# Performance work log

Hardware: AMD Instinct MI355X
Metric: run time of the kernel (lower is better)

The kernel has to match this reference:

```python
import jax, jax.numpy as jnp
import numpy as np

N, T, D, H = 256, 128, 512, 1024


def setup_inputs() -> dict:
    key = jax.random.key(0)
    k_x, k_A, k_Wx, k_Wh, k_Wa = jax.random.split(key, 5)
    x = jax.random.normal(k_x, (N, T, D), dtype=jnp.float32)
    A = jax.random.normal(k_A, (N, H, 4, 4), dtype=jnp.float32)
    Wx = jax.random.normal(k_Wx, (D, 4 * H), dtype=jnp.float32) / np.sqrt(D)
    Wh = jax.random.normal(k_Wh, (H, 4 * H), dtype=jnp.float32) / np.sqrt(H)
    Wattn = jax.random.normal(k_Wa, (H, 4 * H), dtype=jnp.float32) / np.sqrt(H)
    b = jnp.zeros((4 * H,), dtype=jnp.float32)
    return {"x": x, "A": A, "Wx": Wx, "Wh": Wh, "Wattn": Wattn, "b": b}


def _attention_lstm(x, A, Wx, Wh, Wattn, b):
    # A: (N, H, 4, 4) -> flatten spatial to (N, H, 16)
    A_flat = A.reshape(A.shape[0], A.shape[1], -1)
    h0 = A_flat.mean(axis=2)  # (N, H)
    c0 = h0
    Hdim = h0.shape[1]
    scale = 1.0 / jnp.sqrt(jnp.asarray(Hdim, dtype=x.dtype))

    def step(carry, x_t):
        prev_h, prev_c = carry
        # scaled dot-product attention over 16 spatial locations
        scores = jnp.einsum("nh,nhs->ns", prev_h, A_flat) * scale  # (N, 16)
        w = jax.nn.softmax(scores, axis=1)
        attn = jnp.einsum("nhs,ns->nh", A_flat, w)  # (N, H)
        # fused LSTM gates
        a = x_t @ Wx + prev_h @ Wh + attn @ Wattn + b  # (N, 4H)
        i = jax.nn.sigmoid(a[:, 0:Hdim])
        f = jax.nn.sigmoid(a[:, Hdim:2 * Hdim])
        o = jax.nn.sigmoid(a[:, 2 * Hdim:3 * Hdim])
        g = jnp.tanh(a[:, 3 * Hdim:4 * Hdim])
        next_c = f * prev_c + i * g
        next_h = o * jnp.tanh(next_c)
        return (next_h, next_c), next_h

    x_tnd = jnp.swapaxes(x, 0, 1)  # (T, N, D)
    _, h_tnh = jax.lax.scan(step, (h0, c0), x_tnd)
    return jnp.swapaxes(h_tnh, 0, 1)  # (N, T, H)


def reference(x, A, Wx, Wh, Wattn, b):
    return _attention_lstm(x, A, Wx, Wh, Wattn, b)
```

## Files before the change

### kernel.cpp

```cpp
#include <hip/hip_runtime.h>
#include <math.h>

#define NB 256
#define TT 128
#define DD 512
#define HH 1024
#define KHX 1536
#define KFB 2560
#define BK 128
#define NBLK5 256
#define NHALF 128

typedef _Float16 half_t;
typedef _Float16 half8 __attribute__((ext_vector_type(8)));
typedef _Float16 half4v __attribute__((ext_vector_type(4)));
typedef _Float16 half2v __attribute__((ext_vector_type(2)));
typedef float f32x4 __attribute__((ext_vector_type(4)));


__global__ __launch_bounds__(256) void k_trans(const float* __restrict__ src,
        half_t* __restrict__ dst, int kstride, int koff, int nkt) {
    __shared__ half_t tile[64][65];
    int bk = blockIdx.x % nkt;
    int bn = blockIdx.x / nkt;
    int k0 = bk * 64, n0 = bn * 64;
    #pragma unroll
    for (int i = 0; i < 16; ++i) {
        int idx = i * 256 + threadIdx.x;
        int r = idx >> 6, c = idx & 63;
        tile[c][r] = (half_t)src[(size_t)(k0 + r) * 4096 + n0 + c];
    }
    __syncthreads();
    #pragma unroll
    for (int i = 0; i < 16; ++i) {
        int idx = i * 256 + threadIdx.x;
        int r = idx >> 6, c = idx & 63;
        dst[(size_t)(n0 + r) * kstride + koff + k0 + c] = tile[r][c];
    }
}

__global__ __launch_bounds__(256) void k_convX(const float* __restrict__ x,
        half_t* __restrict__ x16) {
    size_t base = ((size_t)blockIdx.x * 256 + threadIdx.x) * 32;
    #pragma unroll
    for (int u = 0; u < 4; ++u) {
        float4 a = ((const float4*)(x + base))[2 * u];
        float4 c = ((const float4*)(x + base))[2 * u + 1];
        half8 p;
        p[0] = (half_t)a.x; p[1] = (half_t)a.y; p[2] = (half_t)a.z; p[3] = (half_t)a.w;
        p[4] = (half_t)c.x; p[5] = (half_t)c.y; p[6] = (half_t)c.z; p[7] = (half_t)c.w;
        ((half8*)(x16 + base))[u] = p;
    }
}

__global__ __launch_bounds__(256) void k_convA2(const float* __restrict__ A,
        half_t* __restrict__ A16, half_t* __restrict__ AsT,
        float* __restrict__ cbuf, half_t* __restrict__ h16) {
    int n = blockIdx.x, tid = threadIdx.x;
    #pragma unroll
    for (int r = 0; r < 4; ++r) {
        int h = tid + r * 256;
        const float4* ap = (const float4*)(A + ((size_t)n * HH + h) * 16);
        float4 v0 = ap[0], v1 = ap[1], v2 = ap[2], v3 = ap[3];
        float a[16];
        a[0]=v0.x; a[1]=v0.y; a[2] =v0.z; a[3] =v0.w;
        a[4]=v1.x; a[5]=v1.y; a[6] =v1.z; a[7] =v1.w;
        a[8]=v2.x; a[9]=v2.y; a[10]=v2.z; a[11]=v2.w;
        a[12]=v3.x; a[13]=v3.y; a[14]=v3.z; a[15]=v3.w;
        float hv = 0.f;
        #pragma unroll
        for (int s = 0; s < 16; ++s) hv += a[s];
        hv *= (1.f / 16.f);
        size_t ci = (size_t)n * HH + h;
        cbuf[ci] = hv;
        h16[ci] = (half_t)hv;
        half8 q0, q1;
        #pragma unroll
        for (int s = 0; s < 8; ++s) { q0[s] = (half_t)a[s]; q1[s] = (half_t)a[s + 8]; }
        *(half8*)(A16 + ci * 16) = q0;
        *(half8*)(A16 + ci * 16 + 8) = q1;
        #pragma unroll
        for (int s = 0; s < 16; ++s)
            AsT[(size_t)n * 16 * HH + (size_t)s * HH + h] = (half_t)a[s];
    }
}

__global__ __launch_bounds__(256) void k_initsc(const half_t* __restrict__ h16,
        const half_t* __restrict__ A16,
        float* __restrict__ sc0, float* __restrict__ sc1, float* __restrict__ sc2) {
    __shared__ float sred[4][16];
    int n = blockIdx.x, tid = threadIdx.x;
    float ps[16];
    #pragma unroll
    for (int s = 0; s < 16; ++s) ps[s] = 0.f;
    #pragma unroll
    for (int r = 0; r < 4; ++r) {
        int h = tid + r * 256;
        size_t ci = (size_t)n * HH + h;
        float hv = (float)h16[ci];
        const half8* ap = (const half8*)(A16 + ci * 16);
        half8 a0 = ap[0], a1 = ap[1];
        #pragma unroll
        for (int s = 0; s < 8; ++s) {
            ps[s]     += hv * (float)a0[s];
            ps[s + 8] += hv * (float)a1[s];
        }
    }
    #pragma unroll
    for (int off = 32; off; off >>= 1)
        #pragma unroll
        for (int s = 0; s < 16; ++s) ps[s] += __shfl_xor(ps[s], off, 64);
    int wave = tid >> 6;
    if ((tid & 63) == 0)
        #pragma unroll
        for (int s = 0; s < 16; ++s) sred[wave][s] = ps[s];
    __syncthreads();
    if (tid < 16)
        sc0[(size_t)n * 16 + tid] =
            sred[0][tid] + sred[1][tid] + sred[2][tid] + sred[3][tid];
    if (tid < 112) {
        int x = 1 + tid / 16, s = tid % 16;
        sc0[((size_t)x * 256 + n) * 16 + s] = 0.f;
    }
    if (tid < 128) {
        int x = tid / 16, s = tid % 16;
        sc1[((size_t)x * 256 + n) * 16 + s] = 0.f;
        sc2[((size_t)x * 256 + n) * 16 + s] = 0.f;
    }
}

__global__ __launch_bounds__(256) void k_gemm_G(const half_t* __restrict__ AsT,
        const half_t* __restrict__ WaT, half_t* __restrict__ G16) {
    __shared__ half_t sAs[16][BK + 8];
    __shared__ half_t sB[4][16][BK + 8];
    int bid = blockIdx.x;
    int n = bid >> 6, jt = bid & 63;
    int j0 = jt * 16;
    int tid = threadIdx.x, wv = tid >> 6, lane = tid & 63;
    f32x4 acc = {};
    int srB = tid >> 2, scB = (tid & 3) * 32;
    int gB = srB >> 4, jcB = srB & 15;
    for (int it = 0; it < HH / BK; ++it) {
        int k0 = it * BK;
        if (tid < 128) {
            int r = tid >> 3, c = (tid & 7) * 16;
            const uint4* sp = (const uint4*)(AsT + (size_t)n * 16 * HH + (size_t)r * HH + k0 + c);
            uint4 u0 = sp[0], u1 = sp[1];
            *(uint4*)&sAs[r][c] = u0;
            *(uint4*)&sAs[r][c + 8] = u1;
        }
        {
            const half_t* src = WaT + ((size_t)(gB * HH + j0 + jcB)) * HH + k0 + scB;
            uint4 u0 = ((const uint4*)src)[0];
            uint4 u1 = ((const uint4*)src)[1];
            uint4 u2 = ((const uint4*)src)[2];
            uint4 u3 = ((const uint4*)src)[3];
            *((uint4*)&sB[gB][jcB][scB])      = u0;
            *((uint4*)&sB[gB][jcB][scB + 8])  = u1;
            *((uint4*)&sB[gB][jcB][scB + 16]) = u2;
            *((uint4*)&sB[gB][jcB][scB + 24]) = u3;
        }
        __syncthreads();
        int row16 = lane & 15, kg = lane >> 4;
        #pragma unroll
        for (int kc = 0; kc < BK / 32; ++kc) {
            half8 bf = *(const half8*)&sB[wv][row16][kc * 32 + kg * 8];
            half8 af = *(const half8*)&sAs[row16][kc * 32 + kg * 8];
            acc = __builtin_amdgcn_mfma_f32_16x16x32_f16(af, bf, acc, 0, 0, 0);
        }
        __syncthreads();
    }
    int col = lane & 15, rbase = (lane >> 4) * 4;
    size_t jf = (size_t)wv * HH + j0 + col;
    half4v o;
    o[0] = (half_t)acc[0]; o[1] = (half_t)acc[1];
    o[2] = (half_t)acc[2]; o[3] = (half_t)acc[3];
    *(half4v*)(G16 + ((size_t)n * 4096 + jf) * 16 + rbase) = o;
}

__global__ __launch_bounds__(256) void k_gemm_XW(const half_t* __restrict__ x16,
        const half_t* __restrict__ WhxT, half_t* __restrict__ XW16) {
    __shared__ half_t sA[128][72];
    __shared__ half_t sB[64][72];
    int bid = blockIdx.x;
    int bm = bid & 255;
    int bj = bid >> 8;
    int row0 = bm * 128;
    int col0 = bj * 64;
    int tid = threadIdx.x, wv = tid >> 6, lane = tid & 63;
    int la = lane & 15, kg = lane >> 4;
    int mh = wv & 1, jh = wv >> 1;
    f32x4 acc[4][2] = {};
    int srA = tid >> 1, scA = (tid & 1) * 32;
    int srB = tid >> 2, scB = (tid & 3) * 16;
    for (int c = 0; c < 8; ++c) {
        {
            const uint4* sp = (const uint4*)(x16 + (size_t)(row0 + srA) * DD + c * 64 + scA);
            uint4 u0 = sp[0], u1 = sp[1];
            *(uint4*)&sA[srA][scA] = u0;
            *(uint4*)&sA[srA][scA + 8] = u1;
        }
        {
            const uint4* sp = (const uint4*)(WhxT + (size_t)(col0 + srB) * KHX + c * 64 + scB);
            *(uint4*)&sB[srB][scB] = sp[0];
        }
        __syncthreads();
        #pragma unroll
        for (int ks = 0; ks < 2; ++ks) {
            half8 b0 = *(const half8*)&sB[jh * 32 + la][ks * 32 + kg * 8];
            half8 b1 = *(const half8*)&sB[jh * 32 + 16 + la][ks * 32 + kg * 8];
            #pragma unroll
            for (int m = 0; m < 4; ++m) {
                half8 af = *(const half8*)&sA[mh * 64 + m * 16 + la][ks * 32 + kg * 8];
                acc[m][0] = __builtin_amdgcn_mfma_f32_16x16x32_f16(af, b0, acc[m][0], 0, 0, 0);
                acc[m][1] = __builtin_amdgcn_mfma_f32_16x16x32_f16(af, b1, acc[m][1], 0, 0, 0);
            }
        }
        __syncthreads();
    }
    __syncthreads();
    half_t (*Cl)[72] = sA;
    #pragma unroll
    for (int m = 0; m < 4; ++m)
        #pragma unroll
        for (int jt = 0; jt < 2; ++jt)
            #pragma unroll
            for (int q = 0; q < 4; ++q) {
                int rl = mh * 64 + m * 16 + kg * 4 + q;
                int cl = jh * 32 + jt * 16 + la;
                Cl[rl][cl] = (half_t)acc[m][jt][q];
            }
    __syncthreads();
    int g = col0 >> 10;
    #pragma unroll
    for (int i = 0; i < 4; ++i) {
        int idx = tid + i * 256;
        int rl = idx >> 3, grp = idx & 7;
        int R = row0 + rl;
        int t = R & 127, nn = R >> 7;
        int mh2 = nn >> 7, nl2 = nn & 127;
        int jb2 = ((col0 & 1023) >> 3) + grp;
        size_t dst = ((((size_t)t * 128 + jb2) * 2 + mh2) * 128 + nl2) * 32 + g * 8;
        *(half8*)(XW16 + dst) = *(const half8*)&Cl[rl][grp * 8];
    }
}


struct StepLds5 {
    half_t W[32][1028];
    union {
        float sm[4][128][16];
        struct {
            float pe[128][33];
            float pad[384];
            float ps[2][128][18];
        } e;
    } u;
};

__device__ __forceinline__ void grid_sync5(int* cnt, int* flag, int inst) {
    __syncthreads();
    if (threadIdx.x == 0) {
        __threadfence();
        int prev = __hip_atomic_fetch_add(cnt, 1, __ATOMIC_RELAXED,
                                          __HIP_MEMORY_SCOPE_AGENT);
        if (prev == NHALF * (inst + 1) - 1) {
            __hip_atomic_store(flag, inst + 1, __ATOMIC_RELAXED,
                               __HIP_MEMORY_SCOPE_AGENT);
        } else {
            int guard = 0;
            while (__hip_atomic_load(flag, __ATOMIC_RELAXED,
                                     __HIP_MEMORY_SCOPE_AGENT) < inst + 1) {
                __builtin_amdgcn_s_sleep(2);
                if (++guard > (1 << 24)) break;
            }
        }
        __threadfence();
    }
    __syncthreads();
}

__global__ __launch_bounds__(512, 1) void k_steps5(
        const half_t* __restrict__ XW16, half_t* __restrict__ h16A,
        half_t* __restrict__ h16B, const half_t* __restrict__ WhxT,
        const half_t* __restrict__ A16, const half_t* __restrict__ G16,
        const float* __restrict__ b, const float* __restrict__ cbuf,
        float* __restrict__ sc0, float* __restrict__ sc1, float* __restrict__ sc2,
        float* __restrict__ out, int* __restrict__ bar) {
    __shared__ StepLds5 L;
    int bid = blockIdx.x;
    int mhalf = bid & 1, jb = bid >> 1;
    int n0 = mhalf * 128;
    int tid = threadIdx.x;
    int wv = tid >> 6, lane = tid & 63;
    int la = lane & 15, kg = lane >> 4;
    int slice = bid & 7;
    int* cnt  = bar + mhalf * 32;
    int* flag = bar + mhalf * 32 + 16;

    {
        int wr = tid >> 4, seg = tid & 15;
        const half_t* wsrc = WhxT + (size_t)((wr >> 3) * HH + jb * 8 + (wr & 7)) * KHX
                           + DD + seg * 64;
        #pragma unroll
        for (int i = 0; i < 8; ++i)
            *(uint4*)&L.W[wr][seg * 64 + i * 8] = ((const uint4*)wsrc)[i];
    }

    int n_l = tid & 127, jg2 = tid >> 7;
    int n = n0 + n_l;
    int jbase = jb * 8 + jg2 * 2;
    half8 gq[4][4];
    #pragma unroll
    for (int g = 0; g < 4; ++g) {
        const half8* gsrc = (const half8*)(G16 + ((size_t)n * 4096 + g * HH + jbase) * 16);
        #pragma unroll
        for (int i = 0; i < 4; ++i) gq[g][i] = gsrc[i];
    }
    half8 aq[4];
    {
        const half8* asrc = (const half8*)(A16 + ((size_t)n * HH + jbase) * 16);
        #pragma unroll
        for (int i = 0; i < 4; ++i) aq[i] = asrc[i];
    }
    float bb[4][2];
    #pragma unroll
    for (int g = 0; g < 4; ++g) {
        bb[g][0] = b[g * HH + jbase];
        bb[g][1] = b[g * HH + jbase + 1];
    }
    float creg[2];
    creg[0] = cbuf[(size_t)n * HH + jbase];
    creg[1] = cbuf[(size_t)n * HH + jbase + 1];

    float* scC = sc0; float* scN = sc1; float* scZ = sc2;
    half_t* h16c = h16A;
    half_t* h16n = h16B;

    half2v xwv[4];
    {
        const half_t* xwp = XW16 + (((size_t)jb * 2 + mhalf) * 128 + n_l) * 32;
        #pragma unroll
        for (int g = 0; g < 4; ++g) xwv[g] = *(const half2v*)(xwp + g * 8 + jg2 * 2);
    }

    for (int t = 0; t < TT; ++t) {
        if (jb < 32) {
            int idx = jb * 512 + tid;
            int sl = idx >> 11, rem = idx & 2047;
            int nn = rem >> 4, s = rem & 15;
            scZ[((size_t)sl * 256 + n0 + nn) * 16 + s] = 0.f;
        }

        {
            const float* p0 = scC + ((size_t)(jg2 * 2) * 256 + n) * 16;
            const float* p1 = scC + ((size_t)(jg2 * 2 + 1) * 256 + n) * 16;
            #pragma unroll
            for (int i = 0; i < 4; ++i) {
                float4 a = ((const float4*)p0)[i];
                float4 c = ((const float4*)p1)[i];
                float4 o;
                o.x = a.x + c.x; o.y = a.y + c.y; o.z = a.z + c.z; o.w = a.w + c.w;
                *(float4*)&L.u.sm[jg2][n_l][4 * i] = o;
            }
        }
        __syncthreads();
        float w16[16];
        {
            float sc[16];
            #pragma unroll
            for (int i = 0; i < 4; ++i) {
                float4 q0 = *(const float4*)&L.u.sm[0][n_l][4 * i];
                float4 q1 = *(const float4*)&L.u.sm[1][n_l][4 * i];
                float4 q2 = *(const float4*)&L.u.sm[2][n_l][4 * i];
                float4 q3 = *(const float4*)&L.u.sm[3][n_l][4 * i];
                sc[4 * i + 0] = q0.x + q1.x + q2.x + q3.x;
                sc[4 * i + 1] = q0.y + q1.y + q2.y + q3.y;
                sc[4 * i + 2] = q0.z + q1.z + q2.z + q3.z;
                sc[4 * i + 3] = q0.w + q1.w + q2.w + q3.w;
            }
            float m = -1e30f;
            #pragma unroll
            for (int s = 0; s < 16; ++s) { sc[s] *= 0.03125f; m = fmaxf(m, sc[s]); }
            float den = 0.f;
            #pragma unroll
            for (int s = 0; s < 16; ++s) { sc[s] = expf(sc[s] - m); den += sc[s]; }
            float inv = 1.f / den;
            #pragma unroll
            for (int s = 0; s < 16; ++s) w16[s] = sc[s] * inv;
        }
        __syncthreads();

        f32x4 acc0 = {}, acc1 = {};
        {
            const half_t* hrow = h16c + (size_t)(n0 + wv * 16 + la) * HH + kg * 8;
            #pragma unroll
            for (int c = 0; c < 32; ++c) {
                half8 af = *(const half8*)(hrow + c * 32);
                half8 b0 = *(const half8*)&L.W[la][c * 32 + kg * 8];
                half8 b1 = *(const half8*)&L.W[16 + la][c * 32 + kg * 8];
                acc0 = __builtin_amdgcn_mfma_f32_16x16x32_f16(af, b0, acc0, 0, 0, 0);
                acc1 = __builtin_amdgcn_mfma_f32_16x16x32_f16(af, b1, acc1, 0, 0, 0);
            }
        }

        #pragma unroll
        for (int q = 0; q < 4; ++q) {
            L.u.e.pe[wv * 16 + kg * 4 + q][la]      = acc0[q];
            L.u.e.pe[wv * 16 + kg * 4 + q][16 + la] = acc1[q];
        }
        __syncthreads();

        float v[4][2];
        #pragma unroll
        for (int g = 0; g < 4; ++g) {
            #pragma unroll
            for (int jj = 0; jj < 2; ++jj) {
                float a0 = 0.f;
                #pragma unroll
                for (int s = 0; s < 16; ++s)
                    a0 += w16[s] * (float)gq[g][jj * 2 + (s >> 3)][s & 7];
                v[g][jj] = L.u.e.pe[n_l][g * 8 + jg2 * 2 + jj] + bb[g][jj]
                         + (float)xwv[g][jj] + a0;
            }
        }
        float hv[2];
        #pragma unroll
        for (int jj = 0; jj < 2; ++jj) {
            float ig = 1.f / (1.f + expf(-v[0][jj]));
            float fg = 1.f / (1.f + expf(-v[1][jj]));
            float og = 1.f / (1.f + expf(-v[2][jj]));
            float gg = tanhf(v[3][jj]);
            float cn = fg * creg[jj] + ig * gg;
            creg[jj] = cn;
            hv[jj] = og * tanhf(cn);
        }
        {
            float2 o2; o2.x = hv[0]; o2.y = hv[1];
            *(float2*)(out + ((size_t)n * TT + t) * HH + jbase) = o2;
            half2v h2; h2[0] = (half_t)hv[0]; h2[1] = (half_t)hv[1];
            *(half2v*)(h16n + (size_t)n * HH + jbase) = h2;
        }
        float p[16];
        #pragma unroll
        for (int s = 0; s < 16; ++s)
            p[s] = hv[0] * (float)aq[s >> 3][s & 7]
                 + hv[1] * (float)aq[2 + (s >> 3)][s & 7];
        int pair = jg2 >> 1;
        if ((jg2 & 1) == 0) {
            #pragma unroll
            for (int s = 0; s < 16; ++s) L.u.e.ps[pair][n_l][s] = p[s];
        }
        __syncthreads();
        if ((jg2 & 1) == 1) {
            #pragma unroll
            for (int s = 0; s < 16; ++s) L.u.e.ps[pair][n_l][s] += p[s];
        }
        __syncthreads();
        #pragma unroll
        for (int i = 0; i < 4; ++i) {
            int slot = tid * 4 + i;
            int nn = slot >> 4, s = slot & 15;
            atomicAdd(scN + ((size_t)slice * 256 + n0 + nn) * 16 + s,
                      L.u.e.ps[0][nn][s] + L.u.e.ps[1][nn][s]);
        }

        if (t + 1 < TT) {
            half2v xwn[4];
            const half_t* xwp = XW16 + ((((size_t)(t + 1) * 128 + jb) * 2 + mhalf) * 128 + n_l) * 32;
            #pragma unroll
            for (int g = 0; g < 4; ++g) xwn[g] = *(const half2v*)(xwp + g * 8 + jg2 * 2);
            grid_sync5(cnt, flag, t);
            #pragma unroll
            for (int g = 0; g < 4; ++g) xwv[g] = xwn[g];
        }
        float* tmp = scC; scC = scN; scN = scZ; scZ = tmp;
        half_t* th = h16c; h16c = h16n; h16n = th;
    }
}


__global__ __launch_bounds__(256) void k_convA(const float* __restrict__ A,
        half_t* __restrict__ A16, half_t* __restrict__ AsT,
        float* __restrict__ cbuf, half_t* __restrict__ h16,
        float* __restrict__ sc0, float* __restrict__ sc1, float* __restrict__ sc2) {
    __shared__ float sred[4][16];
    int n = blockIdx.x, tid = threadIdx.x;
    float ps[16];
    #pragma unroll
    for (int s = 0; s < 16; ++s) ps[s] = 0.f;
    #pragma unroll
    for (int r = 0; r < 4; ++r) {
        int h = tid + r * 256;
        const float4* ap = (const float4*)(A + ((size_t)n * HH + h) * 16);
        float4 v0 = ap[0], v1 = ap[1], v2 = ap[2], v3 = ap[3];
        float a[16];
        a[0]=v0.x; a[1]=v0.y; a[2] =v0.z; a[3] =v0.w;
        a[4]=v1.x; a[5]=v1.y; a[6] =v1.z; a[7] =v1.w;
        a[8]=v2.x; a[9]=v2.y; a[10]=v2.z; a[11]=v2.w;
        a[12]=v3.x; a[13]=v3.y; a[14]=v3.z; a[15]=v3.w;
        float hv = 0.f;
        #pragma unroll
        for (int s = 0; s < 16; ++s) hv += a[s];
        hv *= (1.f / 16.f);
        size_t ci = (size_t)n * HH + h;
        cbuf[ci] = hv;
        h16[ci] = (half_t)hv;
        half8 q0, q1;
        #pragma unroll
        for (int s = 0; s < 8; ++s) { q0[s] = (half_t)a[s]; q1[s] = (half_t)a[s + 8]; }
        *(half8*)(A16 + ci * 16) = q0;
        *(half8*)(A16 + ci * 16 + 8) = q1;
        #pragma unroll
        for (int s = 0; s < 16; ++s)
            AsT[(size_t)n * 16 * HH + (size_t)s * HH + h] = (half_t)a[s];
        #pragma unroll
        for (int s = 0; s < 16; ++s) ps[s] += hv * a[s];
    }
    #pragma unroll
    for (int off = 32; off; off >>= 1)
        #pragma unroll
        for (int s = 0; s < 16; ++s) ps[s] += __shfl_xor(ps[s], off, 64);
    int wave = tid >> 6;
    if ((tid & 63) == 0)
        #pragma unroll
        for (int s = 0; s < 16; ++s) sred[wave][s] = ps[s];
    __syncthreads();
    if (tid < 16) {
        sc0[n * 16 + tid] = sred[0][tid] + sred[1][tid] + sred[2][tid] + sred[3][tid];
        sc1[n * 16 + tid] = 0.f;
        sc2[n * 16 + tid] = 0.f;
    }
}

union LdsS {
    struct {
        half_t sA[32][BK + 8];
        half_t sB[4][16][BK + 8];
    } s;
    float pe[4][32][16];
};

__global__ __launch_bounds__(256) void k_step(const float* __restrict__ x,
        const half_t* __restrict__ h16c, half_t* __restrict__ h16n,
        const half_t* __restrict__ WhxT, const half_t* __restrict__ A16,
        const half_t* __restrict__ G16, const float* __restrict__ b,
        float* __restrict__ cbuf, const float* __restrict__ scC,
        float* __restrict__ scN, float* __restrict__ scZ,
        float* __restrict__ out, int t) {
    __shared__ LdsS L;
    __shared__ float wlds[32][16];
    int bid = blockIdx.x;
    int xcd = bid & 7, slot = bid >> 3;
    int mtile = slot & 7, jtile = slot >> 3;
    int n0 = mtile * 32;
    int j0 = xcd * 128 + jtile * 16;
    int tid = threadIdx.x, wv = tid >> 6, lane = tid & 63;

    if (bid < 16) scZ[bid * 256 + tid] = 0.f;
    if (tid < 32) {
        int n = n0 + tid;
        const float4* sp = (const float4*)(scC + n * 16);
        float4 u0 = sp[0], u1 = sp[1], u2 = sp[2], u3 = sp[3];
        float sc[16] = {u0.x, u0.y, u0.z, u0.w, u1.x, u1.y, u1.z, u1.w,
                        u2.x, u2.y, u2.z, u2.w, u3.x, u3.y, u3.z, u3.w};
        float m = -1e30f;
        #pragma unroll
        for (int s = 0; s < 16; ++s) { sc[s] *= 0.03125f; m = fmaxf(m, sc[s]); }
        float den = 0.f;
        #pragma unroll
        for (int s = 0; s < 16; ++s) { sc[s] = expf(sc[s] - m); den += sc[s]; }
        float inv = 1.f / den;
        #pragma unroll
        for (int s = 0; s < 16; ++s) wlds[tid][s] = sc[s] * inv;
    }

    f32x4 acc[2] = {};
    int srA = tid >> 3, scA = (tid & 7) * 16;
    int srB = tid >> 2, scB = (tid & 3) * 32;
    int gB = srB >> 4, jcB = srB & 15;

    for (int it = 0; it < KHX / BK; ++it) {
        int k0 = it * BK;
        {
            int n = n0 + srA;
            if (k0 < DD) {
                const float* src = x + ((size_t)n * TT + t) * DD + k0 + scA;
                float4 v0 = ((const float4*)src)[0];
                float4 v1 = ((const float4*)src)[1];
                float4 v2 = ((const float4*)src)[2];
                float4 v3 = ((const float4*)src)[3];
                half8 p0, p1;
                p0[0] = (half_t)v0.x; p0[1] = (half_t)v0.y; p0[2] = (half_t)v0.z; p0[3] = (half_t)v0.w;
                p0[4] = (half_t)v1.x; p0[5] = (half_t)v1.y; p0[6] = (half_t)v1.z; p0[7] = (half_t)v1.w;
                p1[0] = (half_t)v2.x; p1[1] = (half_t)v2.y; p1[2] = (half_t)v2.z; p1[3] = (half_t)v2.w;
                p1[4] = (half_t)v3.x; p1[5] = (half_t)v3.y; p1[6] = (half_t)v3.z; p1[7] = (half_t)v3.w;
                *(half8*)&L.s.sA[srA][scA]     = p0;
                *(half8*)&L.s.sA[srA][scA + 8] = p1;
            } else {
                const half_t* srch = h16c + (size_t)n * HH + (k0 - DD) + scA;
                uint4 u0 = ((const uint4*)srch)[0];
                uint4 u1 = ((const uint4*)srch)[1];
                *((uint4*)&L.s.sA[srA][scA])     = u0;
                *((uint4*)&L.s.sA[srA][scA + 8]) = u1;
            }
        }
        {
            const half_t* src = WhxT + ((size_t)(gB * HH + j0 + jcB)) * KHX + k0 + scB;
            uint4 u0 = ((const uint4*)src)[0];
            uint4 u1 = ((const uint4*)src)[1];
            uint4 u2 = ((const uint4*)src)[2];
            uint4 u3 = ((const uint4*)src)[3];
            *((uint4*)&L.s.sB[gB][jcB][scB])      = u0;
            *((uint4*)&L.s.sB[gB][jcB][scB + 8])  = u1;
            *((uint4*)&L.s.sB[gB][jcB][scB + 16]) = u2;
            *((uint4*)&L.s.sB[gB][jcB][scB + 24]) = u3;
        }
        __syncthreads();
        int row16 = lane & 15, kg = lane >> 4;
        #pragma unroll
        for (int kc = 0; kc < BK / 32; ++kc) {
            half8 bf = *(const half8*)&L.s.sB[wv][row16][kc * 32 + kg * 8];
            #pragma unroll
            for (int m = 0; m < 2; ++m) {
                half8 af = *(const half8*)&L.s.sA[row16 + m * 16][kc * 32 + kg * 8];
                acc[m] = __builtin_amdgcn_mfma_f32_16x16x32_f16(af, bf, acc[m], 0, 0, 0);
            }
        }
        __syncthreads();
    }
    {
        int col = lane & 15, rbase = (lane >> 4) * 4;
        #pragma unroll
        for (int m = 0; m < 2; ++m)
            #pragma unroll
            for (int q = 0; q < 4; ++q)
                L.pe[wv][m * 16 + rbase + q][col] = acc[m][q];
    }
    __syncthreads();
    #pragma unroll
    for (int q2 = 0; q2 < 2; ++q2) {
        int idx = tid + q2 * 256;
        int r = idx >> 4, jc = idx & 15;
        int n = n0 + r, j = j0 + jc;
        float wv16[16];
        #pragma unroll
        for (int s = 0; s < 16; ++s) wv16[s] = wlds[r][s];
        float v[4];
        v[0] = L.pe[0][r][jc] + b[j];
        v[1] = L.pe[1][r][jc] + b[HH + j];
        v[2] = L.pe[2][r][jc] + b[2 * HH + j];
        v[3] = L.pe[3][r][jc] + b[3 * HH + j];
        #pragma unroll
        for (int g = 0; g < 4; ++g) {
            const half8* gq = (const half8*)(G16 + ((size_t)n * 4096 + g * HH + j) * 16);
            half8 ga = gq[0], gb2 = gq[1];
            float a0 = 0.f;
            #pragma unroll
            for (int s = 0; s < 8; ++s)
                a0 += wv16[s] * (float)ga[s] + wv16[s + 8] * (float)gb2[s];
            v[g] += a0;
        }
        float ig = 1.f / (1.f + expf(-v[0]));
        float fg = 1.f / (1.f + expf(-v[1]));
        float og = 1.f / (1.f + expf(-v[2]));
        float gg = tanhf(v[3]);
        size_t ci = (size_t)n * HH + j;
        float cp = cbuf[ci];
        float cn = fg * cp + ig * gg;
        cbuf[ci] = cn;
        float hv = og * tanhf(cn);
        out[((size_t)n * TT + t) * HH + j] = hv;
        h16n[ci] = (half_t)hv;
        const half8* ap = (const half8*)(A16 + ci * 16);
        half8 a0 = ap[0], a1 = ap[1];
        float p[16];
        #pragma unroll
        for (int s = 0; s < 8; ++s) { p[s] = hv * (float)a0[s]; p[s + 8] = hv * (float)a1[s]; }
        #pragma unroll
        for (int msk = 1; msk < 16; msk <<= 1)
            #pragma unroll
            for (int s = 0; s < 16; ++s) p[s] += __shfl_xor(p[s], msk, 64);
        float myp = 0.f;
        #pragma unroll
        for (int s = 0; s < 16; ++s) myp = (jc == s) ? p[s] : myp;
        atomicAdd(scN + n * 16 + jc, myp);
    }
}


__global__ __launch_bounds__(256) void fb_wconv(const float* __restrict__ Wx,
        const float* __restrict__ Wh, const float* __restrict__ Wa,
        half_t* __restrict__ WT) {
    __shared__ half_t tile[64][65];
    int bk = blockIdx.x % 40;
    int bn = blockIdx.x / 40;
    int k0 = bk * 64, n0 = bn * 64;
    #pragma unroll
    for (int i = 0; i < 16; ++i) {
        int idx = i * 256 + threadIdx.x;
        int r = idx >> 6, c = idx & 63;
        int k = k0 + r, n = n0 + c;
        float v;
        if (k < DD)            v = Wx[(size_t)k * 4096 + n];
        else if (k < DD + HH)  v = Wh[(size_t)(k - DD) * 4096 + n];
        else                   v = Wa[(size_t)(k - DD - HH) * 4096 + n];
        tile[c][r] = (half_t)v;
    }
    __syncthreads();
    #pragma unroll
    for (int i = 0; i < 16; ++i) {
        int idx = i * 256 + threadIdx.x;
        int r = idx >> 6, c = idx & 63;
        WT[(size_t)(n0 + r) * KFB + k0 + c] = tile[r][c];
    }
}

__global__ __launch_bounds__(256) void fb_init(const float* __restrict__ A,
        float* __restrict__ h0, float* __restrict__ c0) {
    int n = blockIdx.x;
    #pragma unroll
    for (int r = 0; r < 4; ++r) {
        int h = threadIdx.x + r * 256;
        const float4* ap = (const float4*)(A + ((size_t)n * HH + h) * 16);
        float s = 0.f;
        #pragma unroll
        for (int q = 0; q < 4; ++q) {
            float4 v = ap[q];
            s += v.x + v.y + v.z + v.w;
        }
        s *= (1.f / 16.f);
        h0[n * HH + h] = s;
        c0[n * HH + h] = s;
    }
}

__global__ __launch_bounds__(256) void fb_attn(const float* __restrict__ A,
        const float* __restrict__ hprev, long long hstride,
        half_t* __restrict__ h16, half_t* __restrict__ attn16) {
    __shared__ float sh[HH];
    __shared__ float sred[4][16];
    int n = blockIdx.x;
    const float* hp = hprev + (size_t)n * hstride;
    #pragma unroll
    for (int r = 0; r < 4; ++r) {
        int h = threadIdx.x + r * 256;
        float v = hp[h];
        sh[h] = v;
        h16[n * HH + h] = (half_t)v;
    }
    __syncthreads();
    float a[4][16];
    float ps[16];
    #pragma unroll
    for (int s = 0; s < 16; ++s) ps[s] = 0.f;
    #pragma unroll
    for (int r = 0; r < 4; ++r) {
        int h = threadIdx.x + r * 256;
        const float4* ap = (const float4*)(A + ((size_t)n * HH + h) * 16);
        float4 v0 = ap[0], v1 = ap[1], v2 = ap[2], v3 = ap[3];
        a[r][0] = v0.x;  a[r][1] = v0.y;  a[r][2]  = v0.z;  a[r][3]  = v0.w;
        a[r][4] = v1.x;  a[r][5] = v1.y;  a[r][6]  = v1.z;  a[r][7]  = v1.w;
        a[r][8] = v2.x;  a[r][9] = v2.y;  a[r][10] = v2.z;  a[r][11] = v2.w;
        a[r][12] = v3.x; a[r][13] = v3.y; a[r][14] = v3.z;  a[r][15] = v3.w;
        float hh = sh[h];
        #pragma unroll
        for (int s = 0; s < 16; ++s) ps[s] += hh * a[r][s];
    }
    #pragma unroll
    for (int off = 32; off; off >>= 1)
        #pragma unroll
        for (int s = 0; s < 16; ++s) ps[s] += __shfl_xor(ps[s], off, 64);
    int wave = threadIdx.x >> 6;
    if ((threadIdx.x & 63) == 0)
        #pragma unroll
        for (int s = 0; s < 16; ++s) sred[wave][s] = ps[s];
    __syncthreads();
    float sc[16], m = -1e30f;
    #pragma unroll
    for (int s = 0; s < 16; ++s) {
        sc[s] = (sred[0][s] + sred[1][s] + sred[2][s] + sred[3][s]) * 0.03125f;
        m = fmaxf(m, sc[s]);
    }
    float den = 0.f;
    #pragma unroll
    for (int s = 0; s < 16; ++s) { sc[s] = expf(sc[s] - m); den += sc[s]; }
    float inv = 1.f / den;
    #pragma unroll
    for (int r = 0; r < 4; ++r) {
        int h = threadIdx.x + r * 256;
        float acc = 0.f;
        #pragma unroll
        for (int s = 0; s < 16; ++s) acc += a[r][s] * sc[s];
        attn16[n * HH + h] = (half_t)(acc * inv);
    }
}

union LdsFB {
    struct {
        half_t sA[32][BK + 8];
        half_t sB[4][16][BK + 8];
    } s;
    float pe[4][32][16];
};

__global__ __launch_bounds__(256) void fb_gemm(const float* __restrict__ x,
        const half_t* __restrict__ h16, const half_t* __restrict__ attn16,
        const half_t* __restrict__ WT, const float* __restrict__ b,
        float* __restrict__ cbuf, float* __restrict__ out, int t) {
    __shared__ LdsFB L;
    int bid = blockIdx.x;
    int xcd = bid & 7;
    int slot = bid >> 3;
    int mtile = slot & 7;
    int jtile = slot >> 3;
    int m0 = mtile * 32;
    int j0 = xcd * 128 + jtile * 16;
    int tid = threadIdx.x;
    int wv = tid >> 6, lane = tid & 63;
    f32x4 acc[2] = {};
    int srA = tid >> 3, scA = (tid & 7) * 16;
    int srB = tid >> 2, scB = (tid & 3) * 32;
    int gB = srB >> 4, jcB = srB & 15;
    for (int it = 0; it < KFB / BK; ++it) {
        int k0 = it * BK;
        {
            int n = m0 + srA;
            if (k0 < DD) {
                const float* src = x + ((size_t)n * TT + t) * DD + k0 + scA;
                float4 v0 = ((const float4*)src)[0];
                float4 v1 = ((const float4*)src)[1];
                float4 v2 = ((const float4*)src)[2];
                float4 v3 = ((const float4*)src)[3];
                half8 p0, p1;
                p0[0] = (half_t)v0.x; p0[1] = (half_t)v0.y; p0[2] = (half_t)v0.z; p0[3] = (half_t)v0.w;
                p0[4] = (half_t)v1.x; p0[5] = (half_t)v1.y; p0[6] = (half_t)v1.z; p0[7] = (half_t)v1.w;
                p1[0] = (half_t)v2.x; p1[1] = (half_t)v2.y; p1[2] = (half_t)v2.z; p1[3] = (half_t)v2.w;
                p1[4] = (half_t)v3.x; p1[5] = (half_t)v3.y; p1[6] = (half_t)v3.z; p1[7] = (half_t)v3.w;
                *(half8*)&L.s.sA[srA][scA]     = p0;
                *(half8*)&L.s.sA[srA][scA + 8] = p1;
            } else {
                const half_t* srch = (k0 < DD + HH)
                    ? (h16    + (size_t)n * HH + (k0 - DD)      + scA)
                    : (attn16 + (size_t)n * HH + (k0 - DD - HH) + scA);
                uint4 u0 = ((const uint4*)srch)[0];
                uint4 u1 = ((const uint4*)srch)[1];
                *((uint4*)&L.s.sA[srA][scA])     = u0;
                *((uint4*)&L.s.sA[srA][scA + 8]) = u1;
            }
        }
        {
            const half_t* src = WT + ((size_t)(gB * HH + j0 + jcB)) * KFB + k0 + scB;
            uint4 u0 = ((const uint4*)src)[0];
            uint4 u1 = ((const uint4*)src)[1];
            uint4 u2 = ((const uint4*)src)[2];
            uint4 u3 = ((const uint4*)src)[3];
            *((uint4*)&L.s.sB[gB][jcB][scB])      = u0;
            *((uint4*)&L.s.sB[gB][jcB][scB + 8])  = u1;
            *((uint4*)&L.s.sB[gB][jcB][scB + 16]) = u2;
            *((uint4*)&L.s.sB[gB][jcB][scB + 24]) = u3;
        }
        __syncthreads();
        int row16 = lane & 15, kg = lane >> 4;
        #pragma unroll
        for (int kc = 0; kc < BK / 32; ++kc) {
            half8 bf = *(const half8*)&L.s.sB[wv][row16][kc * 32 + kg * 8];
            #pragma unroll
            for (int m = 0; m < 2; ++m) {
                half8 af = *(const half8*)&L.s.sA[row16 + m * 16][kc * 32 + kg * 8];
                acc[m] = __builtin_amdgcn_mfma_f32_16x16x32_f16(af, bf, acc[m], 0, 0, 0);
            }
        }
        __syncthreads();
    }
    {
        int col = lane & 15, rbase = (lane >> 4) * 4;
        #pragma unroll
        for (int m = 0; m < 2; ++m)
            #pragma unroll
            for (int q = 0; q < 4; ++q)
                L.pe[wv][m * 16 + rbase + q][col] = acc[m][q];
    }
    __syncthreads();
    #pragma unroll
    for (int q2 = 0; q2 < 2; ++q2) {
        int idx = tid + q2 * 256;
        int r = idx >> 4, jc = idx & 15;
        int n = m0 + r, j = j0 + jc;
        float vi = L.pe[0][r][jc] + b[j];
        float vf = L.pe[1][r][jc] + b[HH + j];
        float vo = L.pe[2][r][jc] + b[2 * HH + j];
        float vg = L.pe[3][r][jc] + b[3 * HH + j];
        float ig = 1.f / (1.f + expf(-vi));
        float fg = 1.f / (1.f + expf(-vf));
        float og = 1.f / (1.f + expf(-vo));
        float gg = tanhf(vg);
        size_t ci = (size_t)n * HH + j;
        float cp = cbuf[ci];
        float cn = fg * cp + ig * gg;
        cbuf[ci] = cn;
        out[((size_t)n * TT + t) * HH + j] = og * tanhf(cn);
    }
}


extern "C" void kernel_launch(void* const* d_in, const int* in_sizes, int n_in,
                              void* d_out, int out_size, void* d_ws, size_t ws_size,
                              hipStream_t stream) {
    const float* x  = (const float*)d_in[0];
    const float* A  = (const float*)d_in[1];
    const float* Wx = (const float*)d_in[2];
    const float* Wh = (const float*)d_in[3];
    const float* Wa = (const float*)d_in[4];
    const float* b  = (const float*)d_in[5];
    float* out = (float*)d_out;
    char* ws = (char*)d_ws;

    int maxb = 0;
    hipError_t oe = hipOccupancyMaxActiveBlocksPerMultiprocessor(&maxb, k_steps5, 512, 0);
    bool persistent_ok = (oe == hipSuccess && maxb >= 1);

    if (ws_size >= 375439616ULL && persistent_ok) {
        half_t* WhxT = (half_t*)(ws);
        half_t* WaT  = (half_t*)(ws + 12582912);
        half_t* A16  = (half_t*)(ws + 20971520);
        half_t* AsT  = (half_t*)(ws + 29360128);
        half_t* G16  = (half_t*)(ws + 37748736);
        half_t* h16a = (half_t*)(ws + 71303168);
        half_t* h16b = (half_t*)(ws + 71827456);
        float*  cb   = (float*) (ws + 72351744);
        half_t* x16  = (half_t*)(ws + 73449472);
        int*    bar  = (int*)   (ws + 107003904);
        half_t* XW16 = (half_t*)(ws + 107004160);
        float*  sc0  = (float*)(ws + 29360128);
        float*  sc1  = (float*)(ws + 29360128 + 32768);
        float*  sc2  = (float*)(ws + 29360128 + 65536);

        hipLaunchKernelGGL(k_trans, dim3(8 * 64),  dim3(256), 0, stream, Wx, WhxT, KHX, 0,   8);
        hipLaunchKernelGGL(k_trans, dim3(16 * 64), dim3(256), 0, stream, Wh, WhxT, KHX, 512, 16);
        hipLaunchKernelGGL(k_trans, dim3(16 * 64), dim3(256), 0, stream, Wa, WaT,  HH,  0,   16);
        hipLaunchKernelGGL(k_convX, dim3(2048), dim3(256), 0, stream, x, x16);
        hipLaunchKernelGGL(k_convA2, dim3(256), dim3(256), 0, stream, A, A16, AsT, cb, h16a);
        hipLaunchKernelGGL(k_gemm_G, dim3(NB * 64), dim3(256), 0, stream, AsT, WaT, G16);
        hipLaunchKernelGGL(k_gemm_XW, dim3(256 * 64), dim3(256), 0, stream, x16, WhxT, XW16);
        hipLaunchKernelGGL(k_initsc, dim3(256), dim3(256), 0, stream, h16a, A16, sc0, sc1, sc2);
        hipMemsetAsync(bar, 0, 256, stream);
        hipLaunchKernelGGL(k_steps5, dim3(NBLK5), dim3(512), 0, stream,
                           XW16, h16a, h16b, WhxT, A16, G16, b, cb,
                           sc0, sc1, sc2, out, bar);
    } else if (ws_size >= 73449472ULL) {
        half_t* WhxT = (half_t*)(ws);
        half_t* WaT  = (half_t*)(ws + 12582912);
        half_t* A16  = (half_t*)(ws + 20971520);
        half_t* AsT  = (half_t*)(ws + 29360128);
        half_t* G16  = (half_t*)(ws + 37748736);
        half_t* h16a = (half_t*)(ws + 71303168);
        half_t* h16b = (half_t*)(ws + 71827456);
        float*  cb   = (float*) (ws + 72351744);
        float*  sc0  = (float*) (ws + 73400320);
        float*  sc1  = (float*) (ws + 73416704);
        float*  sc2  = (float*) (ws + 73433088);
        float* scb[3] = {sc0, sc1, sc2};

        hipLaunchKernelGGL(k_trans, dim3(8 * 64),  dim3(256), 0, stream, Wx, WhxT, KHX, 0,   8);
        hipLaunchKernelGGL(k_trans, dim3(16 * 64), dim3(256), 0, stream, Wh, WhxT, KHX, 512, 16);
        hipLaunchKernelGGL(k_trans, dim3(16 * 64), dim3(256), 0, stream, Wa, WaT,  HH,  0,   16);
        hipLaunchKernelGGL(k_convA, dim3(256), dim3(256), 0, stream,
                           A, A16, AsT, cb, h16a, sc0, sc1, sc2);
        hipLaunchKernelGGL(k_gemm_G, dim3(NB * 64), dim3(256), 0, stream, AsT, WaT, G16);
        for (int t = 0; t < TT; ++t) {
            float* scC = scb[t % 3];
            float* scN = scb[(t + 1) % 3];
            float* scZ = scb[(t + 2) % 3];
            half_t* h16c = (t & 1) ? h16b : h16a;
            half_t* h16n = (t & 1) ? h16a : h16b;
            hipLaunchKernelGGL(k_step, dim3(512), dim3(256), 0, stream,
                               x, h16c, h16n, WhxT, A16, G16, b, cb, scC, scN, scZ, out, t);
        }
    } else {
        half_t* WT  = (half_t*)ws;
        float*  h0  = (float*)(ws + 20971520);
        float*  cb  = (float*)(ws + 22020096);
        half_t* h16 = (half_t*)(ws + 23068672);
        half_t* a16 = (half_t*)(ws + 23592960);
        hipLaunchKernelGGL(fb_wconv, dim3(2560), dim3(256), 0, stream, Wx, Wh, Wa, WT);
        hipLaunchKernelGGL(fb_init, dim3(256), dim3(256), 0, stream, A, h0, cb);
        for (int t = 0; t < TT; ++t) {
            const float* hp = (t == 0) ? h0 : (out + (size_t)(t - 1) * HH);
            long long hstride = (t == 0) ? (long long)HH : (long long)TT * HH;
            hipLaunchKernelGGL(fb_attn, dim3(256), dim3(256), 0, stream, A, hp, hstride, h16, a16);
            hipLaunchKernelGGL(fb_gemm, dim3(512), dim3(256), 0, stream,
                               x, h16, a16, WT, b, cb, out, t);
        }
    }
}
```

Before: 4.626 ms.

## Replace grid barrier with per-group counters and per-timestep h/score buffers

The persistent step kernel no longer uses a full half-grid barrier each timestep. Each block now bumps one of 32 group counters when done, and readers poll all counters until every group reaches the step target. Hidden states and score partials move to per-timestep slots, which removes ping-pong reuse hazards and the per-step zeroing, at the cost of a much larger workspace and a memset. The XW GEMM is also restructured so each block keeps its x rows in LDS and loops over all column tiles, so it no longer reloads x per tile.

```diff
diff --git a/kernel.cpp b/kernel.cpp
--- a/kernel.cpp
+++ b/kernel.cpp
@@ -8,8 +8,9 @@
 #define KHX 1536
 #define KFB 2560
 #define BK 128
-#define NBLK5 256
-#define NHALF 128
+#define NBLK6 256
+#define SCSLOT 32768
+#define HSLOT (NB * HH)
 
 typedef _Float16 half_t;
 typedef _Float16 half8 __attribute__((ext_vector_type(8)));
@@ -178,116 +179,85 @@
     *(half4v*)(G16 + ((size_t)n * 4096 + jf) * 16 + rbase) = o;
 }
 
-__global__ __launch_bounds__(256) void k_gemm_XW(const half_t* __restrict__ x16,
+__global__ __launch_bounds__(256) void k_gemm_XW2(const half_t* __restrict__ x16,
         const half_t* __restrict__ WhxT, half_t* __restrict__ XW16) {
-    __shared__ half_t sA[128][72];
-    __shared__ half_t sB[64][72];
-    int bid = blockIdx.x;
-    int bm = bid & 255;
-    int bj = bid >> 8;
+    __shared__ half_t sA[128][520];
+    __shared__ half_t sB[128][72];
+    int bm = blockIdx.x;
     int row0 = bm * 128;
-    int col0 = bj * 64;
     int tid = threadIdx.x, wv = tid >> 6, lane = tid & 63;
     int la = lane & 15, kg = lane >> 4;
     int mh = wv & 1, jh = wv >> 1;
-    f32x4 acc[4][2] = {};
-    int srA = tid >> 1, scA = (tid & 1) * 32;
+    {
+        int r = tid >> 1, hseg = tid & 1;
+        const uint4* src = (const uint4*)(x16 + (size_t)(row0 + r) * DD + hseg * 256);
+        #pragma unroll
+        for (int i = 0; i < 16; ++i)
+            *(uint4*)&sA[r][hseg * 256 + i * 8] = src[i];
+    }
+    __syncthreads();
     int srB = tid >> 2, scB = (tid & 3) * 16;
-    for (int c = 0; c < 8; ++c) {
-        {
-            const uint4* sp = (const uint4*)(x16 + (size_t)(row0 + srA) * DD + c * 64 + scA);
-            uint4 u0 = sp[0], u1 = sp[1];
-            *(uint4*)&sA[srA][scA] = u0;
-            *(uint4*)&sA[srA][scA + 8] = u1;
-        }
-        {
-            const uint4* sp = (const uint4*)(WhxT + (size_t)(col0 + srB) * KHX + c * 64 + scB);
-            *(uint4*)&sB[srB][scB] = sp[0];
-        }
-        __syncthreads();
-        #pragma unroll
-        for (int ks = 0; ks < 2; ++ks) {
-            half8 b0 = *(const half8*)&sB[jh * 32 + la][ks * 32 + kg * 8];
-            half8 b1 = *(const half8*)&sB[jh * 32 + 16 + la][ks * 32 + kg * 8];
-            #pragma unroll
-            for (int m = 0; m < 4; ++m) {
-                half8 af = *(const half8*)&sA[mh * 64 + m * 16 + la][ks * 32 + kg * 8];
-                acc[m][0] = __builtin_amdgcn_mfma_f32_16x16x32_f16(af, b0, acc[m][0], 0, 0, 0);
-                acc[m][1] = __builtin_amdgcn_mfma_f32_16x16x32_f16(af, b1, acc[m][1], 0, 0, 0);
-            }
-        }
-        __syncthreads();
-    }
-    __syncthreads();
-    half_t (*Cl)[72] = sA;
-    #pragma unroll
-    for (int m = 0; m < 4; ++m)
-        #pragma unroll
-        for (int jt = 0; jt < 2; ++jt)
-            #pragma unroll
-            for (int q = 0; q < 4; ++q) {
-                int rl = mh * 64 + m * 16 + kg * 4 + q;
-                int cl = jh * 32 + jt * 16 + la;
-                Cl[rl][cl] = (half_t)acc[m][jt][q];
-            }
-    __syncthreads();
-    int g = col0 >> 10;
-    #pragma unroll
-    for (int i = 0; i < 4; ++i) {
-        int idx = tid + i * 256;
-        int rl = idx >> 3, grp = idx & 7;
-        int R = row0 + rl;
-        int t = R & 127, nn = R >> 7;
-        int mh2 = nn >> 7, nl2 = nn & 127;
-        int jb2 = ((col0 & 1023) >> 3) + grp;
-        size_t dst = ((((size_t)t * 128 + jb2) * 2 + mh2) * 128 + nl2) * 32 + g * 8;
-        *(half8*)(XW16 + dst) = *(const half8*)&Cl[rl][grp * 8];
-    }
-}
-
-
-struct StepLds5 {
-    half_t W[32][1028];
-    union {
-        float sm[4][128][16];
-        struct {
-            float pe[128][33];
-            float pad[384];
-            float ps[2][128][18];
-        } e;
-    } u;
-};
-
-__device__ __forceinline__ void grid_sync5(int* cnt, int* flag, int inst) {
-    __syncthreads();
-    if (threadIdx.x == 0) {
-        __threadfence();
-        int prev = __hip_atomic_fetch_add(cnt, 1, __ATOMIC_RELAXED,
-                                          __HIP_MEMORY_SCOPE_AGENT);
-        if (prev == NHALF * (inst + 1) - 1) {
-            __hip_atomic_store(flag, inst + 1, __ATOMIC_RELAXED,
-                               __HIP_MEMORY_SCOPE_AGENT);
-        } else {
-            int guard = 0;
-            while (__hip_atomic_load(flag, __ATOMIC_RELAXED,
-                                     __HIP_MEMORY_SCOPE_AGENT) < inst + 1) {
-                __builtin_amdgcn_s_sleep(2);
-                if (++guard > (1 << 24)) break;
-            }
-        }
-        __threadfence();
-    }
-    __syncthreads();
-}
-
-__global__ __launch_bounds__(512, 1) void k_steps5(
-        const half_t* __restrict__ XW16, half_t* __restrict__ h16A,
-        half_t* __restrict__ h16B, const half_t* __restrict__ WhxT,
-        const half_t* __restrict__ A16, const half_t* __restrict__ G16,
-        const float* __restrict__ b, const float* __restrict__ cbuf,
-        float* __restrict__ sc0, float* __restrict__ sc1, float* __restrict__ sc2,
+    for (int bj = 0; bj < 64; ++bj) {
+        f32x4 acc[4][2] = {};
+        for (int c = 0; c < 8; ++c) {
+            {
+                const uint4* sp = (const uint4*)(WhxT + (size_t)(bj * 64 + srB) * KHX + c * 64 + scB);
+                *(uint4*)&sB[srB][scB] = sp[0];
+            }
+            __syncthreads();
+            #pragma unroll
+            for (int ks = 0; ks < 2; ++ks) {
+                half8 b0 = *(const half8*)&sB[jh * 32 + la][ks * 32 + kg * 8];
+                half8 b1 = *(const half8*)&sB[jh * 32 + 16 + la][ks * 32 + kg * 8];
+                #pragma unroll
+                for (int m = 0; m < 4; ++m) {
+                    half8 af = *(const half8*)&sA[mh * 64 + m * 16 + la][c * 64 + ks * 32 + kg * 8];
+                    acc[m][0] = __builtin_amdgcn_mfma_f32_16x16x32_f16(af, b0, acc[m][0], 0, 0, 0);
+                    acc[m][1] = __builtin_amdgcn_mfma_f32_16x16x32_f16(af, b1, acc[m][1], 0, 0, 0);
+                }
+            }
+            __syncthreads();
+        }
+        #pragma unroll
+        for (int m = 0; m < 4; ++m)
+            #pragma unroll
+            for (int jt = 0; jt < 2; ++jt)
+                #pragma unroll
+                for (int q = 0; q < 4; ++q) {
+                    int rl = mh * 64 + m * 16 + kg * 4 + q;
+                    int cl = jh * 32 + jt * 16 + la;
+                    sB[rl][cl] = (half_t)acc[m][jt][q];
+                }
+        __syncthreads();
+        int col0 = bj * 64;
+        int g = col0 >> 10;
+        #pragma unroll
+        for (int i = 0; i < 4; ++i) {
+            int idx = tid + i * 256;
+            int rl = idx >> 3, grp = idx & 7;
+            int R = row0 + rl;
+            int t = R & 127, nn = R >> 7;
+            int mh2 = nn >> 7, nl2 = nn & 127;
+            int jb2 = ((col0 & 1023) >> 3) + grp;
+            size_t dst = ((((size_t)t * 128 + jb2) * 2 + mh2) * 128 + nl2) * 32 + g * 8;
+            *(half8*)(XW16 + dst) = *(const half8*)&sB[rl][grp * 8];
+        }
+        __syncthreads();
+    }
+}
+
+
+__global__ __launch_bounds__(512, 1) void k_steps6(
+        const half_t* __restrict__ XW16, half_t* __restrict__ hh,
+        const half_t* __restrict__ WhxT, const half_t* __restrict__ A16,
+        const half_t* __restrict__ G16, const float* __restrict__ b,
+        const float* __restrict__ cbuf, float* __restrict__ scr,
         float* __restrict__ out, int* __restrict__ bar) {
-    __shared__ StepLds5 L;
+    __shared__ half_t W[32][1028];
+    __shared__ float sm[4][128][16];
+    __shared__ float pe[128][33];
+    __shared__ float ps[2][128][18];
+
     int bid = blockIdx.x;
     int mhalf = bid & 1, jb = bid >> 1;
     int n0 = mhalf * 128;
@@ -295,8 +265,7 @@
     int wv = tid >> 6, lane = tid & 63;
     int la = lane & 15, kg = lane >> 4;
     int slice = bid & 7;
-    int* cnt  = bar + mhalf * 32;
-    int* flag = bar + mhalf * 32 + 16;
+    int* hcnt = bar + mhalf * 32;
 
     {
         int wr = tid >> 4, seg = tid & 15;
@@ -304,7 +273,7 @@
                            + DD + seg * 64;
         #pragma unroll
         for (int i = 0; i < 8; ++i)
-            *(uint4*)&L.W[wr][seg * 64 + i * 8] = ((const uint4*)wsrc)[i];
+            *(uint4*)&W[wr][seg * 64 + i * 8] = ((const uint4*)wsrc)[i];
     }
 
     int n_l = tid & 127, jg2 = tid >> 7;
@@ -333,35 +302,46 @@
     creg[0] = cbuf[(size_t)n * HH + jbase];
     creg[1] = cbuf[(size_t)n * HH + jbase + 1];
 
-    float* scC = sc0; float* scN = sc1; float* scZ = sc2;
-    half_t* h16c = h16A;
-    half_t* h16n = h16B;
-
-    half2v xwv[4];
-    {
-        const half_t* xwp = XW16 + (((size_t)jb * 2 + mhalf) * 128 + n_l) * 32;
-        #pragma unroll
-        for (int g = 0; g < 4; ++g) xwv[g] = *(const half2v*)(xwp + g * 8 + jg2 * 2);
-    }
+    __threadfence();
+    __syncthreads();
 
     for (int t = 0; t < TT; ++t) {
-        if (jb < 32) {
-            int idx = jb * 512 + tid;
-            int sl = idx >> 11, rem = idx & 2047;
-            int nn = rem >> 4, s = rem & 15;
-            scZ[((size_t)sl * 256 + n0 + nn) * 16 + s] = 0.f;
-        }
-
+        const half_t* hcur = hh + (size_t)t * HSLOT;
+        unsigned* hnext = (unsigned*)(hh + (size_t)(t + 1) * HSLOT);
+        const float* scc = scr + (size_t)t * SCSLOT;
+        float* scn = scr + (size_t)(t + 1) * SCSLOT;
+
+        half2v xwv[4];
         {
-            const float* p0 = scC + ((size_t)(jg2 * 2) * 256 + n) * 16;
-            const float* p1 = scC + ((size_t)(jg2 * 2 + 1) * 256 + n) * 16;
+            const half_t* xwp = XW16 + ((((size_t)t * 128 + jb) * 2 + mhalf) * 128 + n_l) * 32;
+            #pragma unroll
+            for (int g = 0; g < 4; ++g) xwv[g] = *(const half2v*)(xwp + g * 8 + jg2 * 2);
+        }
+
+        if (t > 0) {
+            int tgt = 4 * t;
+            int guard = 0;
+            for (;;) {
+                int v = (lane < 32)
+                    ? __hip_atomic_load(&hcnt[lane], __ATOMIC_RELAXED, __HIP_MEMORY_SCOPE_AGENT)
+                    : tgt;
+                if (__all(v >= tgt)) break;
+                __builtin_amdgcn_s_sleep(2);
+                if (++guard > (1 << 18)) break;
+            }
+        }
+        __builtin_amdgcn_sched_barrier(0);
+
+        {
+            const float* p0 = scc + ((size_t)(jg2 * 2) * 256 + n) * 16;
+            const float* p1 = scc + ((size_t)(jg2 * 2 + 1) * 256 + n) * 16;
             #pragma unroll
             for (int i = 0; i < 4; ++i) {
                 float4 a = ((const float4*)p0)[i];
                 float4 c = ((const float4*)p1)[i];
                 float4 o;
                 o.x = a.x + c.x; o.y = a.y + c.y; o.z = a.z + c.z; o.w = a.w + c.w;
-                *(float4*)&L.u.sm[jg2][n_l][4 * i] = o;
+                *(float4*)&sm[jg2][n_l][4 * i] = o;
             }
         }
         __syncthreads();
@@ -370,10 +350,10 @@
             float sc[16];
             #pragma unroll
             for (int i = 0; i < 4; ++i) {
-                float4 q0 = *(const float4*)&L.u.sm[0][n_l][4 * i];
-                float4 q1 = *(const float4*)&L.u.sm[1][n_l][4 * i];
-                float4 q2 = *(const float4*)&L.u.sm[2][n_l][4 * i];
-                float4 q3 = *(const float4*)&L.u.sm[3][n_l][4 * i];
+                float4 q0 = *(const float4*)&sm[0][n_l][4 * i];
+                float4 q1 = *(const float4*)&sm[1][n_l][4 * i];
+                float4 q2 = *(const float4*)&sm[2][n_l][4 * i];
+                float4 q3 = *(const float4*)&sm[3][n_l][4 * i];
                 sc[4 * i + 0] = q0.x + q1.x + q2.x + q3.x;
                 sc[4 * i + 1] = q0.y + q1.y + q2.y + q3.y;
                 sc[4 * i + 2] = q0.z + q1.z + q2.z + q3.z;
@@ -389,25 +369,25 @@
             #pragma unroll
             for (int s = 0; s < 16; ++s) w16[s] = sc[s] * inv;
         }
-        __syncthreads();
 
         f32x4 acc0 = {}, acc1 = {};
         {
-            const half_t* hrow = h16c + (size_t)(n0 + wv * 16 + la) * HH + kg * 8;
+            const half_t* hrow = hcur + (size_t)(n0 + wv * 16 + la) * HH + kg * 8;
             #pragma unroll
             for (int c = 0; c < 32; ++c) {
                 half8 af = *(const half8*)(hrow + c * 32);
-                half8 b0 = *(const half8*)&L.W[la][c * 32 + kg * 8];
-                half8 b1 = *(const half8*)&L.W[16 + la][c * 32 + kg * 8];
+                half8 b0 = *(const half8*)&W[la][c * 32 + kg * 8];
+                half8 b1 = *(const half8*)&W[16 + la][c * 32 + kg * 8];
                 acc0 = __builtin_amdgcn_mfma_f32_16x16x32_f16(af, b0, acc0, 0, 0, 0);
                 acc1 = __builtin_amdgcn_mfma_f32_16x16x32_f16(af, b1, acc1, 0, 0, 0);
             }
         }
 
+        __syncthreads();
         #pragma unroll
         for (int q = 0; q < 4; ++q) {
-            L.u.e.pe[wv * 16 + kg * 4 + q][la]      = acc0[q];
-            L.u.e.pe[wv * 16 + kg * 4 + q][16 + la] = acc1[q];
+            pe[wv * 16 + kg * 4 + q][la]      = acc0[q];
+            pe[wv * 16 + kg * 4 + q][16 + la] = acc1[q];
         }
         __syncthreads();
 
@@ -420,7 +400,7 @@
                 #pragma unroll
                 for (int s = 0; s < 16; ++s)
                     a0 += w16[s] * (float)gq[g][jj * 2 + (s >> 3)][s & 7];
-                v[g][jj] = L.u.e.pe[n_l][g * 8 + jg2 * 2 + jj] + bb[g][jj]
+                v[g][jj] = pe[n_l][g * 8 + jg2 * 2 + jj] + bb[g][jj]
                          + (float)xwv[g][jj] + a0;
             }
         }
@@ -438,8 +418,10 @@
         {
             float2 o2; o2.x = hv[0]; o2.y = hv[1];
             *(float2*)(out + ((size_t)n * TT + t) * HH + jbase) = o2;
-            half2v h2; h2[0] = (half_t)hv[0]; h2[1] = (half_t)hv[1];
-            *(half2v*)(h16n + (size_t)n * HH + jbase) = h2;
+            union { half2v h2; unsigned u; } cv;
+            cv.h2[0] = (half_t)hv[0]; cv.h2[1] = (half_t)hv[1];
+            __hip_atomic_store(hnext + (((size_t)n * HH + jbase) >> 1), cv.u,
+                               __ATOMIC_RELAXED, __HIP_MEMORY_SCOPE_AGENT);
         }
         float p[16];
         #pragma unroll
@@ -449,33 +431,26 @@
         int pair = jg2 >> 1;
         if ((jg2 & 1) == 0) {
             #pragma unroll
-            for (int s = 0; s < 16; ++s) L.u.e.ps[pair][n_l][s] = p[s];
+            for (int s = 0; s < 16; ++s) ps[pair][n_l][s] = p[s];
         }
         __syncthreads();
         if ((jg2 & 1) == 1) {
             #pragma unroll
-            for (int s = 0; s < 16; ++s) L.u.e.ps[pair][n_l][s] += p[s];
+            for (int s = 0; s < 16; ++s) ps[pair][n_l][s] += p[s];
         }
         __syncthreads();
         #pragma unroll
         for (int i = 0; i < 4; ++i) {
             int slot = tid * 4 + i;
             int nn = slot >> 4, s = slot & 15;
-            atomicAdd(scN + ((size_t)slice * 256 + n0 + nn) * 16 + s,
-                      L.u.e.ps[0][nn][s] + L.u.e.ps[1][nn][s]);
-        }
-
-        if (t + 1 < TT) {
-            half2v xwn[4];
-            const half_t* xwp = XW16 + ((((size_t)(t + 1) * 128 + jb) * 2 + mhalf) * 128 + n_l) * 32;
-            #pragma unroll
-            for (int g = 0; g < 4; ++g) xwn[g] = *(const half2v*)(xwp + g * 8 + jg2 * 2);
-            grid_sync5(cnt, flag, t);
-            #pragma unroll
-            for (int g = 0; g < 4; ++g) xwv[g] = xwn[g];
-        }
-        float* tmp = scC; scC = scN; scN = scZ; scZ = tmp;
-        half_t* th = h16c; h16c = h16n; h16n = th;
+            atomicAdd(scn + ((size_t)slice * 256 + n0 + nn) * 16 + s,
+                      ps[0][nn][s] + ps[1][nn][s]);
+        }
+
+        __syncthreads();
+        if (tid == 0)
+            __hip_atomic_fetch_add(&hcnt[jb >> 2], 1, __ATOMIC_RELAXED,
+                                   __HIP_MEMORY_SCOPE_AGENT);
     }
 }
 
@@ -917,37 +892,37 @@
     char* ws = (char*)d_ws;
 
     int maxb = 0;
-    hipError_t oe = hipOccupancyMaxActiveBlocksPerMultiprocessor(&maxb, k_steps5, 512, 0);
+    hipError_t oe = hipOccupancyMaxActiveBlocksPerMultiprocessor(&maxb, k_steps6, 512, 0);
     bool persistent_ok = (oe == hipSuccess && maxb >= 1);
 
-    if (ws_size >= 375439616ULL && persistent_ok) {
+    if (ws_size >= 460112128ULL && persistent_ok) {
         half_t* WhxT = (half_t*)(ws);
         half_t* WaT  = (half_t*)(ws + 12582912);
         half_t* A16  = (half_t*)(ws + 20971520);
         half_t* AsT  = (half_t*)(ws + 29360128);
         half_t* G16  = (half_t*)(ws + 37748736);
-        half_t* h16a = (half_t*)(ws + 71303168);
-        half_t* h16b = (half_t*)(ws + 71827456);
         float*  cb   = (float*) (ws + 72351744);
         half_t* x16  = (half_t*)(ws + 73449472);
         int*    bar  = (int*)   (ws + 107003904);
         half_t* XW16 = (half_t*)(ws + 107004160);
-        float*  sc0  = (float*)(ws + 29360128);
-        float*  sc1  = (float*)(ws + 29360128 + 32768);
-        float*  sc2  = (float*)(ws + 29360128 + 65536);
+        half_t* HHr  = (half_t*)(ws + 375439616);
+        float*  SCr  = (float*) (ws + 443072768);
+
+        half_t* hh0 = HHr;
 
         hipLaunchKernelGGL(k_trans, dim3(8 * 64),  dim3(256), 0, stream, Wx, WhxT, KHX, 0,   8);
         hipLaunchKernelGGL(k_trans, dim3(16 * 64), dim3(256), 0, stream, Wh, WhxT, KHX, 512, 16);
         hipLaunchKernelGGL(k_trans, dim3(16 * 64), dim3(256), 0, stream, Wa, WaT,  HH,  0,   16);
         hipLaunchKernelGGL(k_convX, dim3(2048), dim3(256), 0, stream, x, x16);
-        hipLaunchKernelGGL(k_convA2, dim3(256), dim3(256), 0, stream, A, A16, AsT, cb, h16a);
+        hipLaunchKernelGGL(k_convA2, dim3(256), dim3(256), 0, stream, A, A16, AsT, cb, hh0);
         hipLaunchKernelGGL(k_gemm_G, dim3(NB * 64), dim3(256), 0, stream, AsT, WaT, G16);
-        hipLaunchKernelGGL(k_gemm_XW, dim3(256 * 64), dim3(256), 0, stream, x16, WhxT, XW16);
-        hipLaunchKernelGGL(k_initsc, dim3(256), dim3(256), 0, stream, h16a, A16, sc0, sc1, sc2);
+        hipLaunchKernelGGL(k_gemm_XW2, dim3(256), dim3(256), 0, stream, x16, WhxT, XW16);
         hipMemsetAsync(bar, 0, 256, stream);
-        hipLaunchKernelGGL(k_steps5, dim3(NBLK5), dim3(512), 0, stream,
-                           XW16, h16a, h16b, WhxT, A16, G16, b, cb,
-                           sc0, sc1, sc2, out, bar);
+        hipMemsetAsync(SCr, 0, 17039360, stream);
+        hipLaunchKernelGGL(k_initsc, dim3(256), dim3(256), 0, stream, hh0, A16,
+                           SCr, SCr + SCSLOT, SCr + 2 * SCSLOT);
+        hipLaunchKernelGGL(k_steps6, dim3(NBLK6), dim3(512), 0, stream,
+                           XW16, HHr, WhxT, A16, G16, b, cb, SCr, out, bar);
     } else if (ws_size >= 73449472ULL) {
         half_t* WhxT = (half_t*)(ws);
         half_t* WaT  = (half_t*)(ws + 12582912);
```

Result: no change. 4.635 ms (+0.2%).
